# Kernel optimization log

Hardware: AMD Instinct MI355X
Metric: run time of the kernel (lower is better)

Reference implementation:

```python
import jax, jax.numpy as jnp
import numpy as np
import math

EMB_DIM = 1024
NUM_HEADS = 16
D_H = EMB_DIM // NUM_HEADS
B, S = 2, 2048


def setup_inputs() -> dict:
    key = jax.random.key(0)
    ks = jax.random.split(key, 6)
    limit = math.sqrt(6.0 / (EMB_DIM + D_H))  # xavier_uniform per head
    x = jax.random.normal(ks[0], (B, S, EMB_DIM), dtype=jnp.float32)
    Wq = jax.random.uniform(ks[1], (NUM_HEADS, EMB_DIM, D_H), jnp.float32, -limit, limit)
    Wk = jax.random.uniform(ks[2], (NUM_HEADS, EMB_DIM, D_H), jnp.float32, -limit, limit)
    Wv = jax.random.uniform(ks[3], (NUM_HEADS, EMB_DIM, D_H), jnp.float32, -limit, limit)
    bq = jnp.zeros((NUM_HEADS, D_H), jnp.float32)
    bk = jnp.zeros((NUM_HEADS, D_H), jnp.float32)
    bv = jnp.zeros((NUM_HEADS, D_H), jnp.float32)
    limo = math.sqrt(6.0 / (EMB_DIM + EMB_DIM))
    W_O = jax.random.uniform(ks[4], (EMB_DIM, EMB_DIM), jnp.float32, -limo, limo)
    causal_mask = jnp.tril(jnp.ones((S, S), jnp.float32))
    padding_mask = jnp.zeros((B, S), jnp.bool_)  # all-False: nothing padded
    return {"x": x, "Wq": Wq, "bq": bq, "Wk": Wk, "bk": bk, "Wv": Wv,
            "bv": bv, "W_O": W_O, "causal_mask": causal_mask,
            "padding_mask": padding_mask}


def reference(x, Wq, bq, Wk, bk, Wv, bv, W_O, causal_mask, padding_mask):
    # Per-head projections, vectorized over heads: [B,S,E] x [H,E,D] -> [B,H,S,D]
    Q = jnp.einsum('bse,hed->bhsd', x, Wq) + bq[None, :, None, :]
    K = jnp.einsum('bse,hed->bhsd', x, Wk) + bk[None, :, None, :]
    V = jnp.einsum('bse,hed->bhsd', x, Wv) + bv[None, :, None, :]
    scores = jnp.einsum('bhsd,bhtd->bhst', Q, K) / math.sqrt(D_H)
    neg_inf = jnp.float32(-jnp.inf)
    scores = jnp.where(causal_mask[None, None, :, :] == 0, neg_inf, scores)
    scores = jnp.where(padding_mask[:, None, None, :], neg_inf, scores)
    attn = jax.nn.softmax(scores, axis=-1)
    out = jnp.einsum('bhst,bhtd->bhsd', attn, V)  # [B,H,S,D]
    # concat heads in order (dim=-1) -> [B,S,H*D]
    x_concat = out.transpose(0, 2, 1, 3).reshape(B, S, EMB_DIM)
    return x_concat @ W_O
```

## Files before the change

kernel.cpp:

```cpp
#include <hip/hip_runtime.h>
#include <hip/hip_bf16.h>


typedef __hip_bfloat16 bf16;
typedef __attribute__((ext_vector_type(8))) short bfrag;
typedef __attribute__((ext_vector_type(4))) float f32x4;
typedef __attribute__((ext_vector_type(16))) float f32x16;
typedef __attribute__((ext_vector_type(4))) short short4v;

#define MFMA16(a, b, c) __builtin_amdgcn_mfma_f32_16x16x32_bf16(a, b, c, 0, 0, 0)
#define MFMA32(a, b, c) __builtin_amdgcn_mfma_f32_32x32x16_bf16(a, b, c, 0, 0, 0)

__device__ __forceinline__ unsigned pk2(float a, float b) {
  union { __hip_bfloat162 h; unsigned u; } w;
  w.h = __float22bfloat162_rn(make_float2(a, b));
  return w.u;
}

__device__ __forceinline__ void gload16(const bf16* g, bf16* l) {
  __builtin_amdgcn_global_load_lds(
      (const __attribute__((address_space(1))) void*)(g),
      (__attribute__((address_space(3))) void*)(l), 16, 0, 0);
}

__device__ __forceinline__ void barrier_raw() {
  asm volatile("" ::: "memory");
  __builtin_amdgcn_s_barrier();
  asm volatile("" ::: "memory");
}

__global__ __launch_bounds__(256) void prep_all(const float* __restrict__ x,
                                                const float* __restrict__ Wq,
                                                const float* __restrict__ Wk,
                                                const float* __restrict__ Wv,
                                                const float* __restrict__ Wo,
                                                bf16* __restrict__ xb,
                                                bf16* __restrict__ WqkvT,
                                                bf16* __restrict__ WoT) {
  __shared__ bf16 tile[64][80];
  int id = blockIdx.x;
  int t = threadIdx.x;
  if (id < 2048) {
    int i = id * 2048 + t * 8;
    float4 a = *(const float4*)(x + i);
    float4 b = *(const float4*)(x + i + 4);
    union { bf16 h[8]; bfrag v; } tmp;
    tmp.h[0] = __float2bfloat16(a.x); tmp.h[1] = __float2bfloat16(a.y);
    tmp.h[2] = __float2bfloat16(a.z); tmp.h[3] = __float2bfloat16(a.w);
    tmp.h[4] = __float2bfloat16(b.x); tmp.h[5] = __float2bfloat16(b.y);
    tmp.h[6] = __float2bfloat16(b.z); tmp.h[7] = __float2bfloat16(b.w);
    *(bfrag*)(xb + i) = tmp.v;
    return;
  }
  int wid = id - 2048;
  const float* src;
  bf16* dst;
  int srcld, dstld, r0, c0;
  if (wid < 768) {
    int w = wid >> 8, h = (wid >> 4) & 15;
    r0 = (wid & 15) * 64; c0 = 0;
    src = ((w == 0) ? Wq : (w == 1) ? Wk : Wv) + (long)h * 1024 * 64;
    dst = WqkvT + ((long)w * 1024 + h * 64) * 1024;
    srcld = 64; dstld = 1024;
  } else {
    int j = wid - 768;
    c0 = (j & 15) * 64; r0 = (j >> 4) * 64;
    src = Wo; dst = WoT;
    srcld = 1024; dstld = 1024;
  }
  int lr = t >> 3, lc = (t & 7) << 3;
#pragma unroll
  for (int p = 0; p < 2; ++p) {
    int r = lr + p * 32;
    const float* s = src + (long)(r0 + r) * srcld + c0 + lc;
    union { bf16 h8[8]; bfrag v; } tmp;
#pragma unroll
    for (int j = 0; j < 8; ++j) tmp.h8[j] = __float2bfloat16(s[j]);
    *(bfrag*)(&tile[r][lc]) = tmp.v;
  }
  __syncthreads();
#pragma unroll
  for (int p = 0; p < 2; ++p) {
    int c = lr + p * 32;
    union { bf16 h8[8]; bfrag v; } tmp;
#pragma unroll
    for (int j = 0; j < 8; ++j) tmp.h8[j] = tile[lc + j][c];
    *(bfrag*)(dst + (long)(c0 + c) * dstld + r0 + lc) = tmp.v;
  }
}

__global__ __launch_bounds__(512, 2) void gemm_qkv128(const bf16* __restrict__ xb,
                                                      const bf16* __restrict__ WT,
                                                      const float* __restrict__ bq,
                                                      const float* __restrict__ bk,
                                                      const float* __restrict__ bv,
                                                      bf16* __restrict__ Q,
                                                      bf16* __restrict__ K_,
                                                      bf16* __restrict__ Vt) {
  extern __shared__ bf16 lds[];
  int id = blockIdx.x;
  int xcd = id & 7, idx = id >> 3;
  int tile = xcd * 32 + idx;
  int mt = tile & 15, nt = tile >> 4;
  int m0 = mt * 256, n0 = nt * 192;

  int t = threadIdx.x;
  int wave = t >> 6, lane = t & 63, quad = lane >> 4, col = lane & 15;
  int wm = wave >> 2, wn = wave & 3;

  int schunk = 8 * ((t & 7) ^ ((t >> 3) & 7));
  const bf16* aSrc = xb + (long)(m0 + (t >> 3)) * 1024 + schunk;
  const bf16* bSrc = WT + (long)(n0 + (t >> 3)) * 1024 + schunk;
  int wv512 = wave * 512;

  int xoff0 = (quad * 8) ^ ((col & 7) << 3);
  const bf16* aRdB = lds + wm * 8192 + col * 64;
  const bf16* bRdB = lds + 32768 + (wn * 48 + col) * 64;

  f32x4 acc[8][3] = {};

#define STA(BUF, HALF, G, KS)                                                  \
  gload16(aSrc + (long)((HALF)*128 + (G)*64) * 1024 + (KS)*64,                 \
          lds + (BUF)*16384 + (HALF)*8192 + (G)*4096 + wv512)
#define STB(BUF, G, KS)                                                        \
  gload16(bSrc + (long)((G)*64) * 1024 + (KS)*64,                              \
          lds + 32768 + (BUF)*12288 + (G)*4096 + wv512)

#define PHASE(BUF, MH, KC, STAGES, VMW)                                        \
  {                                                                            \
    int xk = xoff0 ^ ((KC)*32);                                                \
    bfrag ra[4], rb[3];                                                        \
    _Pragma("unroll") for (int u = 0; u < 4; ++u)                              \
      ra[u] = *(const bfrag*)(aRdB + (BUF)*16384 + (MH)*4096 + u * 1024 + xk); \
    _Pragma("unroll") for (int c2 = 0; c2 < 3; ++c2)                           \
      rb[c2] = *(const bfrag*)(bRdB + (BUF)*12288 + c2 * 1024 + xk);           \
    STAGES;                                                                    \
    VMW;                                                                       \
    barrier_raw();                                                             \
    __builtin_amdgcn_s_setprio(1);                                             \
    _Pragma("unroll") for (int ni = 0; ni < 3; ++ni)                           \
      _Pragma("unroll") for (int mi2 = 0; mi2 < 4; ++mi2)                      \
        acc[(MH)*4 + mi2][ni] = MFMA16(ra[mi2], rb[ni], acc[(MH)*4 + mi2][ni]);\
    __builtin_amdgcn_s_setprio(0);                                             \
    barrier_raw();                                                             \
  }

#define VM2 asm volatile("s_waitcnt vmcnt(2)" ::: "memory")
#define NOVM

  STA(0, 0, 0, 0); STA(0, 1, 0, 0); STA(0, 0, 1, 0); STA(0, 1, 1, 0);
  STB(0, 0, 0); STB(0, 1, 0); STB(0, 2, 0);
  STA(1, 0, 0, 1); STA(1, 1, 0, 1);
  VM2;
  barrier_raw();

  for (int it = 0; it < 8; ++it) {
    int ksB = 2 * it + 1;
    int kA  = (it < 7) ? 2 * it + 2 : 14;
    int ksB2 = (it < 7) ? 2 * it + 3 : 15;
    PHASE(0, 0, 0, { STA(1, 0, 1, ksB); STA(1, 1, 1, ksB); }, NOVM);
    PHASE(0, 0, 1, { STB(1, 0, ksB); STB(1, 1, ksB); }, NOVM);
    PHASE(0, 1, 0, { STB(1, 2, ksB); }, NOVM);
    PHASE(0, 1, 1, { STA(0, 0, 0, kA); STA(0, 1, 0, kA); }, VM2);
    PHASE(1, 0, 0, { STA(0, 0, 1, kA); STA(0, 1, 1, kA); }, NOVM);
    PHASE(1, 0, 1, { STB(0, 0, kA); STB(0, 1, kA); }, NOVM);
    PHASE(1, 1, 0, { STB(0, 2, kA); }, NOVM);
    PHASE(1, 1, 1, { STA(1, 0, 0, ksB2); STA(1, 1, 0, ksB2); }, VM2);
  }
#undef PHASE
#undef STA
#undef STB
#undef VM2
#undef NOVM

  asm volatile("s_waitcnt vmcnt(0)" ::: "memory");
  barrier_raw();

  const float SC2 = 0.18033688f;
  int b = m0 >> 11, sbase = m0 & 2047;

  if (n0 < 1920) {
#pragma unroll
    for (int ni = 0; ni < 3; ++ni) {
      int n = wn * 48 + ni * 16 + col;
      int ng = n0 + n;
      int s01 = ng >> 10;
      float bvv = s01 ? bk[ng & 1023] : bq[ng & 1023];
      float qsv = s01 ? 1.0f : SC2;
#pragma unroll
      for (int mi = 0; mi < 8; ++mi) {
        int mrow = wm * 128 + mi * 16 + quad * 4;
#pragma unroll
        for (int r = 0; r < 4; ++r)
          lds[(mrow + r) * 200 + n] = __float2bfloat16((acc[mi][ni][r] + bvv) * qsv);
      }
    }
    barrier_raw();
    int row = t >> 1, half = t & 1;
#pragma unroll
    for (int s = 0; s < 12; ++s) {
      int cl = 96 * half + 8 * s;
      int ng = n0 + cl;
      int s01 = ng >> 10, within = ng & 1023;
      int h = within >> 6, d = within & 63;
      bf16* dst = s01 ? K_ : Q;
      *(bfrag*)(dst + ((long)((b << 4) + h) * 2048 + sbase + row) * 64 + d) =
          *(const bfrag*)(lds + row * 200 + cl);
    }
  } else if (n0 == 1920) {
#pragma unroll
    for (int ni = 0; ni < 3; ++ni) {
      int n = wn * 48 + ni * 16 + col;
      int ng = n0 + n;
      if (ng < 2048) {
        float bvv = bk[ng & 1023];
#pragma unroll
        for (int mi = 0; mi < 8; ++mi) {
          int mrow = wm * 128 + mi * 16 + quad * 4;
#pragma unroll
          for (int r = 0; r < 4; ++r)
            lds[(mrow + r) * 136 + n] = __float2bfloat16(acc[mi][ni][r] + bvv);
        }
      } else {
        int vn = n - 128;
        float bvv = bv[ng & 1023];
#pragma unroll
        for (int mi = 0; mi < 8; ++mi) {
          int m = wm * 128 + mi * 16 + quad * 4;
          union { unsigned u[2]; unsigned long long ull; } pkd;
          pkd.u[0] = pk2(acc[mi][ni][0] + bvv, acc[mi][ni][1] + bvv);
          pkd.u[1] = pk2(acc[mi][ni][2] + bvv, acc[mi][ni][3] + bvv);
          *(unsigned long long*)(lds + 34816 + vn * 264 + m) = pkd.ull;
        }
      }
    }
    barrier_raw();
#pragma unroll
    for (int p = 0; p < 8; ++p) {
      int u = p * 512 + t;
      int row = u >> 4, cl = (u & 15) * 8;
      int within = (n0 + cl) & 1023;
      int h = within >> 6, d = within & 63;
      *(bfrag*)(K_ + ((long)((b << 4) + h) * 2048 + sbase + row) * 64 + d) =
          *(const bfrag*)(lds + row * 136 + cl);
    }
#pragma unroll
    for (int p = 0; p < 4; ++p) {
      int u = p * 512 + t;
      int vn = u >> 5, seg = (u & 31) * 8;
      int within = (n0 + 128 + vn) & 1023;
      int h = within >> 6, d = within & 63;
      *(bfrag*)(Vt + ((long)((b << 4) + h) * 64 + d) * 2048 + sbase + seg) =
          *(const bfrag*)(lds + 34816 + vn * 264 + seg);
    }
  } else {
#pragma unroll
    for (int ni = 0; ni < 3; ++ni) {
      int n = wn * 48 + ni * 16 + col;
      int ng = n0 + n;
      float bvv = bv[ng & 1023];
#pragma unroll
      for (int mi = 0; mi < 8; ++mi) {
        int m = wm * 128 + mi * 16 + quad * 4;
        union { unsigned u[2]; unsigned long long ull; } pkd;
        pkd.u[0] = pk2(acc[mi][ni][0] + bvv, acc[mi][ni][1] + bvv);
        pkd.u[1] = pk2(acc[mi][ni][2] + bvv, acc[mi][ni][3] + bvv);
        *(unsigned long long*)(lds + n * 264 + m) = pkd.ull;
      }
    }
    barrier_raw();
#pragma unroll
    for (int p = 0; p < 12; ++p) {
      int u = p * 512 + t;
      int rn = u >> 5, seg = (u & 31) * 8;
      int within = (n0 + rn) & 1023;
      int h = within >> 6, d = within & 63;
      *(bfrag*)(Vt + ((long)((b << 4) + h) * 64 + d) * 2048 + sbase + seg) =
          *(const bfrag*)(lds + rn * 264 + seg);
    }
  }
}

__global__ __launch_bounds__(256) void gemm_out(const bf16* __restrict__ O,
                                                const bf16* __restrict__ Bt,
                                                float* __restrict__ Cf) {
  const int K = 1024;
  __shared__ bf16 As[2][128 * 64];
  __shared__ bf16 Bs[2][64 * 64];
  int id = blockIdx.x;
  int xcd = id & 7, sw = id >> 3;
  int m0 = ((xcd << 2) | (sw & 3)) * 128;
  int n0 = (sw >> 2) * 64;
  int t = threadIdx.x;
  int wave = t >> 6, lane = t & 63, quad = lane >> 4, col = lane & 15;
  int wr = (wave >> 1) * 64, wc = (wave & 1) * 32;
  f32x4 acc[2][4] = {};

  int schunk = 8 * ((t & 7) ^ ((t >> 3) & 7));
  int ob = m0 >> 11;
  const bf16* AsrcB = O + (long)ob * 2097152 + (long)((m0 & 2047) + (t >> 3)) * 64 + schunk;
  const bf16* BsrcB = Bt + (long)(n0 + (t >> 3)) * K + schunk;
  int wv = wave * 512;
  int xoff0 = (quad * 8) ^ ((col & 7) << 3);

#define OUT_STAGE(bi, k0n)                                                 \
  {                                                                        \
    long ko = ((long)((k0n) >> 6)) * 131072;                               \
    _Pragma("unroll") for (int i = 0; i < 4; ++i)                          \
      gload16(AsrcB + ko + (long)(32 * i) * 64, &As[bi][i * 2048 + wv]);   \
    _Pragma("unroll") for (int i = 0; i < 2; ++i)                          \
      gload16(BsrcB + (k0n) + (long)(32 * i) * K, &Bs[bi][i * 2048 + wv]); \
  }

  OUT_STAGE(0, 0);
  __syncthreads();
  for (int k0 = 0; k0 < K; k0 += 64) {
    int cur = (k0 >> 6) & 1;
    if (k0 + 64 < K) OUT_STAGE(cur ^ 1, k0 + 64);
#pragma unroll
    for (int kc = 0; kc < 2; ++kc) {
      int xk = xoff0 ^ (kc * 32);
      bfrag ra[4], rb[2];
#pragma unroll
      for (int i = 0; i < 4; ++i)
        ra[i] = *(const bfrag*)(&As[cur][(wr + 16 * i + col) * 64 + xk]);
#pragma unroll
      for (int c = 0; c < 2; ++c)
        rb[c] = *(const bfrag*)(&Bs[cur][(wc + 16 * c + col) * 64 + xk]);
#pragma unroll
      for (int c = 0; c < 2; ++c)
#pragma unroll
        for (int i = 0; i < 4; ++i) acc[c][i] = MFMA16(ra[i], rb[c], acc[c][i]);
    }
    __syncthreads();
  }
#undef OUT_STAGE

#pragma unroll
  for (int c = 0; c < 2; ++c) {
    int n = n0 + wc + 16 * c + col;
#pragma unroll
    for (int i = 0; i < 4; ++i)
#pragma unroll
      for (int r = 0; r < 4; ++r) {
        int m = m0 + wr + 16 * i + quad * 4 + r;
        Cf[(long)m * 1024 + n] = acc[c][i][r];
      }
  }
}

__global__ __launch_bounds__(256) void attn_kernel(const bf16* __restrict__ Q,
                                                   const bf16* __restrict__ K_,
                                                   const bf16* __restrict__ Vt,
                                                   bf16* __restrict__ O) {
  int id = blockIdx.x;
  int xcd = id & 7, jj = id >> 3;
  int qt = 31 - (jj >> 2);
  int bh = ((jj & 3) << 3) | xcd;

  __shared__ bf16 Ks[128][72];
  __shared__ bf16 Vs[64][136];

  int t = threadIdx.x, wave = t >> 6, lane = t & 63;
  int qh = wave >> 1, jh = wave & 1, hi = lane >> 5, l5 = lane & 31;

  int krow = t >> 3, kg = (t & 7) * 8;
  int vrow = t >> 4, vg = (t & 15) * 8;
  const bf16* KuBase = K_ + (long)bh * 2048 * 64;
  const bf16* VuBase = Vt + (long)bh * 64 * 2048;
  int kL = krow * 64 + kg;
  int vL = vrow * 2048 + vg;

  int q0 = qt * 64;
  int nj = (qt >> 1) + 1;
  int qi = q0 + 32 * qh + l5;

  bfrag qa[4];
  const bf16* qp = Q + ((long)bh * 2048 + q0 + 32 * qh + l5) * 64 + hi * 8;
#pragma unroll
  for (int kd = 0; kd < 4; ++kd) qa[kd] = *(const bfrag*)(qp + kd * 16);

  f32x16 o0, o1;
  float lsum = 0.f;
#pragma unroll
  for (int r = 0; r < 16; ++r) { o0[r] = 0.f; o1[r] = 0.f; }

  bfrag kreg[4], vreg[4];
#pragma unroll
  for (int i = 0; i < 4; ++i) {
    kreg[i] = *(const bfrag*)(KuBase + kL + i * 2048);
    vreg[i] = *(const bfrag*)(VuBase + vL + i * 32768);
  }

  for (int jt = 0; jt < nj; ++jt) {
    int j0 = jt * 128;
    __syncthreads();
#pragma unroll
    for (int i = 0; i < 4; ++i) {
      *(bfrag*)(&Ks[krow + 32 * i][kg]) = kreg[i];
      *(bfrag*)(&Vs[vrow + 16 * i][vg]) = vreg[i];
    }
    int jn = (jt + 1 < nj) ? j0 + 128 : j0;
    const bf16* kp = KuBase + (long)jn * 64;
    const bf16* vp = VuBase + jn;
#pragma unroll
    for (int i = 0; i < 4; ++i) {
      kreg[i] = *(const bfrag*)(kp + kL + i * 2048);
      vreg[i] = *(const bfrag*)(vp + vL + i * 32768);
    }
    __syncthreads();

    bool lastT = (jt == nj - 1);
    if (lastT && jh == 1 && ((qt & 1) == 0)) continue;

    f32x16 s0, s1;
#pragma unroll
    for (int r = 0; r < 16; ++r) { s0[r] = 0.f; s1[r] = 0.f; }
    __builtin_amdgcn_s_setprio(1);
#pragma unroll
    for (int kd = 0; kd < 4; ++kd) {
      bfrag ka0 = *(const bfrag*)(&Ks[jh * 64 + l5][kd * 16 + hi * 8]);
      bfrag ka1 = *(const bfrag*)(&Ks[jh * 64 + 32 + l5][kd * 16 + hi * 8]);
      s0 = MFMA32(ka0, qa[kd], s0);
      s1 = MFMA32(ka1, qa[kd], s1);
    }
    __builtin_amdgcn_s_setprio(0);

    unsigned g[2][4][2];
#pragma unroll
    for (int jb = 0; jb < 2; ++jb) {
      float pv[16];
      float ls = 0.f;
#pragma unroll
      for (int r = 0; r < 16; ++r) {
        int jl = (r & 3) + 8 * (r >> 2) + 4 * hi;
        int j = j0 + jh * 64 + jb * 32 + jl;
        float sv = jb ? s1[r] : s0[r];
        float p = __builtin_amdgcn_exp2f(sv);
        if (lastT) p = (j <= qi) ? p : 0.f;
        ls += p;
        pv[r] = p;
      }
      lsum += ls;
#pragma unroll
      for (int gg = 0; gg < 4; ++gg) {
        g[jb][gg][0] = pk2(pv[4 * gg], pv[4 * gg + 1]);
        g[jb][gg][1] = pk2(pv[4 * gg + 2], pv[4 * gg + 3]);
      }
    }

    __builtin_amdgcn_s_setprio(1);
#pragma unroll
    for (int jb = 0; jb < 2; ++jb) {
#pragma unroll
      for (int c = 0; c < 2; ++c) {
        unsigned a0 = g[jb][2 * c][0], a1 = g[jb][2 * c][1];
        unsigned b0 = g[jb][2 * c + 1][0], b1 = g[jb][2 * c + 1][1];
        asm("v_permlane32_swap_b32 %0, %1" : "+v"(a0), "+v"(b0));
        asm("v_permlane32_swap_b32 %0, %1" : "+v"(a1), "+v"(b1));
        union { unsigned u[4]; bfrag f; } pf;
        pf.u[0] = a0;
        pf.u[1] = a1;
        pf.u[2] = b0;
        pf.u[3] = b1;
        int kk = jh * 64 + jb * 32 + c * 16 + hi * 8;
        bfrag av0 = *(const bfrag*)(&Vs[l5][kk]);
        bfrag av1 = *(const bfrag*)(&Vs[32 + l5][kk]);
        o0 = MFMA32(av0, pf.f, o0);
        o1 = MFMA32(av1, pf.f, o1);
      }
    }
    __builtin_amdgcn_s_setprio(0);
  }

  lsum += __shfl_xor(lsum, 32, 64);

  __syncthreads();
  float* Osc = (float*)&Ks[0][0];
  float* Lsc = (float*)&Vs[0][0];
  bf16* Of = (bf16*)((char*)&Vs[0][0] + 512);
  int q = 32 * qh + l5;
  if (jh == 1) {
#pragma unroll
    for (int r = 0; r < 16; ++r) {
      int d = (r & 3) + 8 * (r >> 2) + 4 * hi;
      Osc[q * 68 + d] = o0[r];
      Osc[q * 68 + 32 + d] = o1[r];
    }
    if (hi == 0) Lsc[q] = lsum;
  }
  __syncthreads();
  if (jh == 0) {
    float inv = 1.f / (lsum + Lsc[q]);
#pragma unroll
    for (int r = 0; r < 16; ++r) {
      int d = (r & 3) + 8 * (r >> 2) + 4 * hi;
      Of[q * 72 + d] = __float2bfloat16((o0[r] + Osc[q * 68 + d]) * inv);
      Of[q * 72 + 32 + d] = __float2bfloat16((o1[r] + Osc[q * 68 + 32 + d]) * inv);
    }
  }
  __syncthreads();
  int row = t >> 2, off = (t & 3) * 16;
  bf16* po = O + ((long)bh * 2048 + q0 + row) * 64 + off;
  *(bfrag*)(po) = *(const bfrag*)(&Of[row * 72 + off]);
  *(bfrag*)(po + 8) = *(const bfrag*)(&Of[row * 72 + off + 8]);
}

extern "C" void kernel_launch(void* const* d_in, const int* in_sizes, int n_in,
                              void* d_out, int out_size, void* d_ws, size_t ws_size,
                              hipStream_t stream) {
  const float* x  = (const float*)d_in[0];
  const float* Wq = (const float*)d_in[1];
  const float* bq = (const float*)d_in[2];
  const float* Wk = (const float*)d_in[3];
  const float* bk = (const float*)d_in[4];
  const float* Wv = (const float*)d_in[5];
  const float* bv = (const float*)d_in[6];
  const float* Wo = (const float*)d_in[7];
  float* out = (float*)d_out;

  bf16* ws = (bf16*)d_ws;
  const long MB1 = 1 << 20;
  bf16* WqkvT = ws + 0 * MB1;
  bf16* WoT   = ws + 3 * MB1;
  bf16* Q     = ws + 4 * MB1;
  bf16* K_    = ws + 8 * MB1;
  bf16* Vt    = ws + 12 * MB1;
  bf16* O     = ws + 16 * MB1;
  bf16* xb    = ws + 20 * MB1;

  prep_all<<<3072, 256, 0, stream>>>(x, Wq, Wk, Wv, Wo, xb, WqkvT, WoT);
  gemm_qkv128<<<256, 512, 114688, stream>>>(xb, WqkvT, bq, bk, bv, Q, K_, Vt);
  attn_kernel<<<1024, 256, 0, stream>>>(Q, K_, Vt, O);
  gemm_out<<<512, 256, 0, stream>>>(O, WoT, out);
}
```

Before: 186.4 us.

## Split KV range for longest causal query tiles and merge partials in combine kernel

The eight longest query tiles per head (qt 24–31) are split into two KV-range halves, each processed by its own block that writes unnormalized fp32 partial outputs and row sums to workspace. A new combine kernel adds the halves, normalizes, and writes bf16 O. The aim is to shorten the critical path of the causal-attention tail by balancing work across more blocks. In exchange it adds a kernel launch, extra fp32 global traffic, and reuses the xb/WqkvT workspace regions for the partials.

```diff
diff --git a/kernel.cpp b/kernel.cpp
--- a/kernel.cpp
+++ b/kernel.cpp
@@ -352,10 +352,24 @@
 __global__ __launch_bounds__(256) void attn_kernel(const bf16* __restrict__ Q,
                                                    const bf16* __restrict__ K_,
                                                    const bf16* __restrict__ Vt,
-                                                   bf16* __restrict__ O) {
+                                                   bf16* __restrict__ O,
+                                                   float* __restrict__ Opart,
+                                                   float* __restrict__ Lpart) {
   int id = blockIdx.x;
-  int xcd = id & 7, jj = id >> 3;
-  int qt = 31 - (jj >> 2);
+  int xcd = id & 7;
+  int qt, part, isSplit, jj;
+  if (id < 512) {
+    jj = id >> 3;
+    qt = 31 - (jj >> 3);
+    part = (jj >> 2) & 1;
+    isSplit = 1;
+  } else {
+    int u = id - 512;
+    jj = u >> 3;
+    qt = 23 - (jj >> 2);
+    part = 0;
+    isSplit = 0;
+  }
   int bh = ((jj & 3) << 3) | xcd;
 
   __shared__ bf16 Ks[128][72];
@@ -372,7 +386,9 @@
   int vL = vrow * 2048 + vg;
 
   int q0 = qt * 64;
-  int nj = (qt >> 1) + 1;
+  int njf = (qt >> 1) + 1;
+  int b0 = 0, b1 = njf;
+  if (isSplit) { int h2 = njf >> 1; b0 = part ? h2 : 0; b1 = part ? njf : h2; }
   int qi = q0 + 32 * qh + l5;
 
   bfrag qa[4];
@@ -386,13 +402,17 @@
   for (int r = 0; r < 16; ++r) { o0[r] = 0.f; o1[r] = 0.f; }
 
   bfrag kreg[4], vreg[4];
-#pragma unroll
-  for (int i = 0; i < 4; ++i) {
-    kreg[i] = *(const bfrag*)(KuBase + kL + i * 2048);
-    vreg[i] = *(const bfrag*)(VuBase + vL + i * 32768);
-  }
-
-  for (int jt = 0; jt < nj; ++jt) {
+  {
+    const bf16* kp0 = KuBase + (long)(b0 * 128) * 64;
+    const bf16* vp0 = VuBase + b0 * 128;
+#pragma unroll
+    for (int i = 0; i < 4; ++i) {
+      kreg[i] = *(const bfrag*)(kp0 + kL + i * 2048);
+      vreg[i] = *(const bfrag*)(vp0 + vL + i * 32768);
+    }
+  }
+
+  for (int jt = b0; jt < b1; ++jt) {
     int j0 = jt * 128;
     __syncthreads();
 #pragma unroll
@@ -400,7 +420,7 @@
       *(bfrag*)(&Ks[krow + 32 * i][kg]) = kreg[i];
       *(bfrag*)(&Vs[vrow + 16 * i][vg]) = vreg[i];
     }
-    int jn = (jt + 1 < nj) ? j0 + 128 : j0;
+    int jn = (jt + 1 < b1) ? j0 + 128 : j0;
     const bf16* kp = KuBase + (long)jn * 64;
     const bf16* vp = VuBase + jn;
 #pragma unroll
@@ -410,7 +430,7 @@
     }
     __syncthreads();
 
-    bool lastT = (jt == nj - 1);
+    bool lastT = (jt == njf - 1);
     if (lastT && jh == 1 && ((qt & 1) == 0)) continue;
 
     f32x16 s0, s1;
@@ -455,14 +475,14 @@
 #pragma unroll
       for (int c = 0; c < 2; ++c) {
         unsigned a0 = g[jb][2 * c][0], a1 = g[jb][2 * c][1];
-        unsigned b0 = g[jb][2 * c + 1][0], b1 = g[jb][2 * c + 1][1];
-        asm("v_permlane32_swap_b32 %0, %1" : "+v"(a0), "+v"(b0));
-        asm("v_permlane32_swap_b32 %0, %1" : "+v"(a1), "+v"(b1));
+        unsigned b0u = g[jb][2 * c + 1][0], b1u = g[jb][2 * c + 1][1];
+        asm("v_permlane32_swap_b32 %0, %1" : "+v"(a0), "+v"(b0u));
+        asm("v_permlane32_swap_b32 %0, %1" : "+v"(a1), "+v"(b1u));
         union { unsigned u[4]; bfrag f; } pf;
         pf.u[0] = a0;
         pf.u[1] = a1;
-        pf.u[2] = b0;
-        pf.u[3] = b1;
+        pf.u[2] = b0u;
+        pf.u[3] = b1u;
         int kk = jh * 64 + jb * 32 + c * 16 + hi * 8;
         bfrag av0 = *(const bfrag*)(&Vs[l5][kk]);
         bfrag av1 = *(const bfrag*)(&Vs[32 + l5][kk]);
@@ -477,8 +497,7 @@
 
   __syncthreads();
   float* Osc = (float*)&Ks[0][0];
-  float* Lsc = (float*)&Vs[0][0];
-  bf16* Of = (bf16*)((char*)&Vs[0][0] + 512);
+  float* Lsc = (float*)((char*)&Ks[0][0] + 17408);
   int q = 32 * qh + l5;
   if (jh == 1) {
 #pragma unroll
@@ -490,20 +509,63 @@
     if (hi == 0) Lsc[q] = lsum;
   }
   __syncthreads();
-  if (jh == 0) {
-    float inv = 1.f / (lsum + Lsc[q]);
-#pragma unroll
-    for (int r = 0; r < 16; ++r) {
-      int d = (r & 3) + 8 * (r >> 2) + 4 * hi;
-      Of[q * 72 + d] = __float2bfloat16((o0[r] + Osc[q * 68 + d]) * inv);
-      Of[q * 72 + 32 + d] = __float2bfloat16((o1[r] + Osc[q * 68 + 32 + d]) * inv);
-    }
-  }
-  __syncthreads();
-  int row = t >> 2, off = (t & 3) * 16;
-  bf16* po = O + ((long)bh * 2048 + q0 + row) * 64 + off;
-  *(bfrag*)(po) = *(const bfrag*)(&Of[row * 72 + off]);
-  *(bfrag*)(po + 8) = *(const bfrag*)(&Of[row * 72 + off + 8]);
+
+  if (!isSplit) {
+    bf16* Of = (bf16*)&Vs[0][0];
+    if (jh == 0) {
+      float inv = 1.f / (lsum + Lsc[q]);
+#pragma unroll
+      for (int r = 0; r < 16; ++r) {
+        int d = (r & 3) + 8 * (r >> 2) + 4 * hi;
+        Of[q * 72 + d] = __float2bfloat16((o0[r] + Osc[q * 68 + d]) * inv);
+        Of[q * 72 + 32 + d] = __float2bfloat16((o1[r] + Osc[q * 68 + 32 + d]) * inv);
+      }
+    }
+    __syncthreads();
+    int row = t >> 2, off = (t & 3) * 16;
+    bf16* po = O + ((long)bh * 2048 + q0 + row) * 64 + off;
+    *(bfrag*)(po) = *(const bfrag*)(&Of[row * 72 + off]);
+    *(bfrag*)(po + 8) = *(const bfrag*)(&Of[row * 72 + off + 8]);
+  } else {
+    int pidx = (((31 - qt) << 5) | bh) * 2 + part;
+    float* Ff = (float*)&Vs[0][0];
+    if (jh == 0) {
+      float lt = lsum + Lsc[q];
+#pragma unroll
+      for (int r = 0; r < 16; ++r) {
+        int d = (r & 3) + 8 * (r >> 2) + 4 * hi;
+        Ff[q * 68 + d] = o0[r] + Osc[q * 68 + d];
+        Ff[q * 68 + 32 + d] = o1[r] + Osc[q * 68 + 32 + d];
+      }
+      if (hi == 0) Lpart[pidx * 64 + q] = lt;
+    }
+    __syncthreads();
+    float* po = Opart + (long)pidx * 4096;
+    int row = t >> 2, sg = (t & 3) * 16;
+#pragma unroll
+    for (int u2 = 0; u2 < 4; ++u2)
+      *(float4*)(po + row * 64 + sg + u2 * 4) = *(const float4*)(&Ff[row * 68 + sg + u2 * 4]);
+  }
+}
+
+__global__ __launch_bounds__(256) void attn_combine(const float* __restrict__ Opart,
+                                                    const float* __restrict__ Lpart,
+                                                    bf16* __restrict__ O) {
+  int c = blockIdx.x;
+  int qt = 24 + (c >> 5), bh = c & 31;
+  int base = (((31 - qt) << 5) | bh) * 2;
+  const float* pa = Opart + (long)base * 4096;
+  const float* pb = pa + 4096;
+  int t = threadIdx.x;
+  int q = t >> 2, sg = (t & 3) * 16;
+  float inv = 1.f / (Lpart[base * 64 + q] + Lpart[(base + 1) * 64 + q]);
+  union { bf16 h[16]; bfrag v[2]; } o;
+#pragma unroll
+  for (int u = 0; u < 16; ++u)
+    o.h[u] = __float2bfloat16((pa[q * 64 + sg + u] + pb[q * 64 + sg + u]) * inv);
+  bf16* po = O + ((long)bh * 2048 + qt * 64 + q) * 64 + sg;
+  *(bfrag*)(po) = o.v[0];
+  *(bfrag*)(po + 8) = o.v[1];
 }
 
 extern "C" void kernel_launch(void* const* d_in, const int* in_sizes, int n_in,
@@ -529,8 +591,12 @@
   bf16* O     = ws + 16 * MB1;
   bf16* xb    = ws + 20 * MB1;
 
+  float* Opart = (float*)xb;
+  float* Lpart = (float*)WqkvT;
+
   prep_all<<<3072, 256, 0, stream>>>(x, Wq, Wk, Wv, Wo, xb, WqkvT, WoT);
   gemm_qkv128<<<256, 512, 114688, stream>>>(xb, WqkvT, bq, bk, bv, Q, K_, Vt);
-  attn_kernel<<<1024, 256, 0, stream>>>(Q, K_, Vt, O);
+  attn_kernel<<<1280, 256, 0, stream>>>(Q, K_, Vt, O, Opart, Lpart);
+  attn_combine<<<256, 256, 0, stream>>>(Opart, Lpart, O);
   gemm_out<<<512, 256, 0, stream>>>(O, WoT, out);
 }
```

Result: slower. 193.7 us (+3.9%).
